# Optimization experiments

Measured on AMD Instinct MI355X. Metric: run time of the kernel, lower is better.

The kernel has to match this reference:

```python
import jax, jax.numpy as jnp
import numpy as np

NUM_GRAPHS = 512  # number of distinct graph ids in batch


def _gcn_agg(x, batch):
    # mm(block_full_adj, x) == per-graph sum broadcast back to nodes
    sums = jax.ops.segment_sum(x, batch, num_segments=NUM_GRAPHS)
    return sums[batch]


def setup_inputs() -> dict:
    key = jax.random.key(0)
    ks = jax.random.split(key, 8)
    N, D = 100000, 128
    H = 2 * D
    x = jax.random.normal(ks[0], (N, D), dtype=jnp.float32)
    batch = jnp.sort(jax.random.randint(ks[1], (N,), 0, NUM_GRAPHS)).astype(jnp.int64)
    s = 0.05
    W1 = jax.random.normal(ks[2], (D, H), dtype=jnp.float32) * s
    b1 = jax.random.normal(ks[3], (H,), dtype=jnp.float32) * s
    W2 = jax.random.normal(ks[4], (H, H), dtype=jnp.float32) * s
    b2 = jax.random.normal(ks[5], (H,), dtype=jnp.float32) * s
    Wc = jax.random.normal(ks[6], (H, 1), dtype=jnp.float32) * s
    bc = jax.random.normal(ks[7], (1,), dtype=jnp.float32) * s
    return {"x": x, "batch": batch, "W1": W1, "b1": b1, "W2": W2, "b2": b2, "Wc": Wc, "bc": bc}


def reference(x, batch, W1, b1, W2, b2, Wc, bc):
    h = jax.nn.relu(_gcn_agg(x, batch) @ W1 + b1)          # GCN layer 1
    h = jax.nn.relu(_gcn_agg(h, batch) @ W2 + b2)          # GCN layer 2
    c = h @ Wc + bc                                         # confidence head
    sp = jax.nn.softplus(c)
    return sp / (1.0 + sp)
```

## Files before the change

kernel.cpp:

```cpp
#include <hip/hip_runtime.h>
#include <math.h>

#define NUM_GRAPHS 512
#define D 128
#define HDIM 256

__global__ __launch_bounds__(256) void graph_mlp(
    const float* __restrict__ x,
    const int*   __restrict__ batch32,
    const float* __restrict__ W1, const float* __restrict__ b1,
    const float* __restrict__ W2, const float* __restrict__ b2,
    const float* __restrict__ Wc, const float* __restrict__ bc,
    float* __restrict__ cval, int* __restrict__ flagOut, int N)
{
    const int g   = blockIdx.x;
    const int tid = threadIdx.x;

    __shared__ int    sIs64;
    __shared__ int    sStart, sEnd;
    __shared__ float4 part[256];
    __shared__ float  sS[D];
    __shared__ float  sH[HDIM];
    __shared__ float  sRed[4];
    __shared__ int    sWave[4];

    {
        int cap = N < 8192 ? N : 8192;
        int local = 0x7fffffff;
        for (int i = tid; i < cap; i += 256) {
            if (batch32[i] != 0) { local = i; break; }
        }
        for (int off = 32; off > 0; off >>= 1)
            local = min(local, __shfl_down(local, off, 64));
        if ((tid & 63) == 0) sWave[tid >> 6] = local;
        __syncthreads();
        if (tid == 0) {
            int j = min(min(sWave[0], sWave[1]), min(sWave[2], sWave[3]));
            int is64 = 0;
            if (j != 0x7fffffff && j + 1 < N && batch32[j + 1] == 0) is64 = 1;
            sIs64 = is64;
            if (g == 0) *flagOut = is64;
        }
        __syncthreads();
    }
    const int is64 = sIs64;
    const long long* batch64 = (const long long*)batch32;

    if (tid < 2) {
        int target = g + tid;
        int lo = 0, hi = N;
        while (lo < hi) {
            int m = (lo + hi) >> 1;
            long long v = is64 ? batch64[m] : (long long)batch32[m];
            if (v < (long long)target) lo = m + 1; else hi = m;
        }
        if (tid == 0) sStart = lo; else sEnd = lo;
    }
    __syncthreads();
    const int start = sStart, end = sEnd;
    const float cnt = (float)(end - start);

    const int r  = tid >> 5;
    const int c4 = tid & 31;
    float4 acc = make_float4(0.f, 0.f, 0.f, 0.f);
    const float4* x4 = (const float4*)x;
    for (int row = start + r; row < end; row += 8) {
        float4 v = x4[row * 32 + c4];
        acc.x += v.x; acc.y += v.y; acc.z += v.z; acc.w += v.w;
    }
    part[tid] = acc;
    __syncthreads();
    for (int s = 4; s >= 1; s >>= 1) {
        if (r < s) {
            float4 o = part[tid + s * 32];
            float4 m = part[tid];
            m.x += o.x; m.y += o.y; m.z += o.z; m.w += o.w;
            part[tid] = m;
        }
        __syncthreads();
    }
    if (tid < 32) {
        float4 v = part[tid];
        sS[tid * 4 + 0] = v.x;
        sS[tid * 4 + 1] = v.y;
        sS[tid * 4 + 2] = v.z;
        sS[tid * 4 + 3] = v.w;
    }
    __syncthreads();

    float a1 = b1[tid];
    #pragma unroll 8
    for (int k = 0; k < D; ++k)
        a1 = fmaf(sS[k], W1[k * HDIM + tid], a1);
    sH[tid] = fmaxf(a1, 0.f) * cnt;
    __syncthreads();

    float a2 = b2[tid];
    #pragma unroll 8
    for (int k = 0; k < HDIM; ++k)
        a2 = fmaf(sH[k], W2[k * HDIM + tid], a2);
    float h2 = fmaxf(a2, 0.f);
    float v = h2 * Wc[tid];
    for (int off = 32; off > 0; off >>= 1)
        v += __shfl_down(v, off, 64);
    if ((tid & 63) == 0) sRed[tid >> 6] = v;
    __syncthreads();
    if (tid == 0) {
        float cc = sRed[0] + sRed[1] + sRed[2] + sRed[3] + bc[0];
        float m  = fmaxf(cc, 0.f);
        float sp = m + log1pf(expf(-fabsf(cc)));
        cval[g] = sp / (1.f + sp);
    }
}

__global__ __launch_bounds__(256) void scatter_out(
    const int* __restrict__ batch32, const int* __restrict__ flag,
    const float* __restrict__ cval, float* __restrict__ out, int N)
{
    const int is64 = *flag;
    const long long* batch64 = (const long long*)batch32;
    int i = blockIdx.x * 256 + threadIdx.x;
    if (i < N) {
        int g = is64 ? (int)batch64[i] : batch32[i];
        out[i] = cval[g];
    }
}

extern "C" void kernel_launch(void* const* d_in, const int* in_sizes, int n_in,
                              void* d_out, int out_size, void* d_ws, size_t ws_size,
                              hipStream_t stream)
{
    const float* x   = (const float*)d_in[0];
    const int*   bat = (const int*)d_in[1];
    const float* W1  = (const float*)d_in[2];
    const float* b1  = (const float*)d_in[3];
    const float* W2  = (const float*)d_in[4];
    const float* b2  = (const float*)d_in[5];
    const float* Wc  = (const float*)d_in[6];
    const float* bc  = (const float*)d_in[7];
    float* out = (float*)d_out;
    const int N = in_sizes[0] / D;

    float* cval = (float*)d_ws;
    int*   flag = (int*)((char*)d_ws + NUM_GRAPHS * sizeof(float));

    graph_mlp<<<NUM_GRAPHS, 256, 0, stream>>>(x, bat, W1, b1, W2, b2, Wc, bc,
                                              cval, flag, N);
    scatter_out<<<(N + 255) / 256, 256, 0, stream>>>(bat, flag, cval, out, N);
}
```

Measured before the change: 118.3 us.

## Split segment sum across blocks and batch MLP over several graphs per block

The segment sum now runs in its own kernel, which splits each graph's rows across K blocks to expose more parallelism and writes partial sums to workspace. A second kernel reduces the partials for GPB graphs per block, so each W1/W2 weight load is reused across four graphs, and writes the output directly over each graph's contiguous row range instead of using a separate scatter kernel. The probe that detects 32- versus 64-bit batch indices now scans fewer entries. The cost is a workspace round trip for the partials and fewer blocks (128) doing the MLP stage.

```diff
diff --git a/kernel.cpp b/kernel.cpp
--- a/kernel.cpp
+++ b/kernel.cpp
@@ -4,67 +4,75 @@
 #define NUM_GRAPHS 512
 #define D 128
 #define HDIM 256
-
-__global__ __launch_bounds__(256) void graph_mlp(
-    const float* __restrict__ x,
-    const int*   __restrict__ batch32,
-    const float* __restrict__ W1, const float* __restrict__ b1,
-    const float* __restrict__ W2, const float* __restrict__ b2,
-    const float* __restrict__ Wc, const float* __restrict__ bc,
-    float* __restrict__ cval, int* __restrict__ flagOut, int N)
-{
-    const int g   = blockIdx.x;
+#define K 4
+#define GPB 4
+
+#define DETECT_IS64(batch32, N, tid, sWave, sIs64)                         \
+    {                                                                      \
+        int cap = (N) < 1024 ? (N) : 1024;                                 \
+        int local = 0x7fffffff;                                            \
+        for (int i = (tid); i < cap; i += 256)                             \
+            if ((batch32)[i] != 0) { local = i; break; }                   \
+        for (int off = 32; off > 0; off >>= 1)                             \
+            local = min(local, __shfl_down(local, off, 64));               \
+        if (((tid) & 63) == 0) (sWave)[(tid) >> 6] = local;                \
+        __syncthreads();                                                   \
+        if ((tid) == 0) {                                                  \
+            int j = min(min((sWave)[0], (sWave)[1]),                       \
+                        min((sWave)[2], (sWave)[3]));                      \
+            (sIs64) = (j != 0x7fffffff && j + 1 < (N) &&                   \
+                       (batch32)[j + 1] == 0) ? 1 : 0;                     \
+        }                                                                  \
+        __syncthreads();                                                   \
+    }
+
+__device__ __forceinline__ int lower_bound_g(const int* batch32, int is64,
+                                             int N, int target)
+{
+    const long long* batch64 = (const long long*)batch32;
+    int lo = 0, hi = N;
+    while (lo < hi) {
+        int m = (lo + hi) >> 1;
+        long long v = is64 ? batch64[m] : (long long)batch32[m];
+        if (v < (long long)target) lo = m + 1; else hi = m;
+    }
+    return lo;
+}
+
+__global__ __launch_bounds__(256) void seg_sum(
+    const float* __restrict__ x, const int* __restrict__ batch32,
+    float4* __restrict__ partial4, int N)
+{
+    const int blk = blockIdx.x;
+    const int g   = blk / K;
+    const int k   = blk % K;
     const int tid = threadIdx.x;
 
     __shared__ int    sIs64;
+    __shared__ int    sWave[4];
     __shared__ int    sStart, sEnd;
     __shared__ float4 part[256];
-    __shared__ float  sS[D];
-    __shared__ float  sH[HDIM];
-    __shared__ float  sRed[4];
-    __shared__ int    sWave[4];
-
-    {
-        int cap = N < 8192 ? N : 8192;
-        int local = 0x7fffffff;
-        for (int i = tid; i < cap; i += 256) {
-            if (batch32[i] != 0) { local = i; break; }
-        }
-        for (int off = 32; off > 0; off >>= 1)
-            local = min(local, __shfl_down(local, off, 64));
-        if ((tid & 63) == 0) sWave[tid >> 6] = local;
-        __syncthreads();
-        if (tid == 0) {
-            int j = min(min(sWave[0], sWave[1]), min(sWave[2], sWave[3]));
-            int is64 = 0;
-            if (j != 0x7fffffff && j + 1 < N && batch32[j + 1] == 0) is64 = 1;
-            sIs64 = is64;
-            if (g == 0) *flagOut = is64;
-        }
-        __syncthreads();
-    }
+
+    DETECT_IS64(batch32, N, tid, sWave, sIs64);
     const int is64 = sIs64;
-    const long long* batch64 = (const long long*)batch32;
 
     if (tid < 2) {
-        int target = g + tid;
-        int lo = 0, hi = N;
-        while (lo < hi) {
-            int m = (lo + hi) >> 1;
-            long long v = is64 ? batch64[m] : (long long)batch32[m];
-            if (v < (long long)target) lo = m + 1; else hi = m;
-        }
+        int lo = lower_bound_g(batch32, is64, N, g + tid);
         if (tid == 0) sStart = lo; else sEnd = lo;
     }
     __syncthreads();
+
     const int start = sStart, end = sEnd;
-    const float cnt = (float)(end - start);
+    const int n   = end - start;
+    const int per = (n + K - 1) / K;
+    const int r0  = start + k * per;
+    const int r1  = min(r0 + per, end);
 
     const int r  = tid >> 5;
     const int c4 = tid & 31;
     float4 acc = make_float4(0.f, 0.f, 0.f, 0.f);
     const float4* x4 = (const float4*)x;
-    for (int row = start + r; row < end; row += 8) {
+    for (int row = r0 + r; row < r1; row += 8) {
         float4 v = x4[row * 32 + c4];
         acc.x += v.x; acc.y += v.y; acc.z += v.z; acc.w += v.w;
     }
@@ -79,50 +87,103 @@
         }
         __syncthreads();
     }
-    if (tid < 32) {
-        float4 v = part[tid];
-        sS[tid * 4 + 0] = v.x;
-        sS[tid * 4 + 1] = v.y;
-        sS[tid * 4 + 2] = v.z;
-        sS[tid * 4 + 3] = v.w;
-    }
-    __syncthreads();
-
-    float a1 = b1[tid];
-    #pragma unroll 8
-    for (int k = 0; k < D; ++k)
-        a1 = fmaf(sS[k], W1[k * HDIM + tid], a1);
-    sH[tid] = fmaxf(a1, 0.f) * cnt;
-    __syncthreads();
-
-    float a2 = b2[tid];
-    #pragma unroll 8
-    for (int k = 0; k < HDIM; ++k)
-        a2 = fmaf(sH[k], W2[k * HDIM + tid], a2);
-    float h2 = fmaxf(a2, 0.f);
-    float v = h2 * Wc[tid];
-    for (int off = 32; off > 0; off >>= 1)
-        v += __shfl_down(v, off, 64);
-    if ((tid & 63) == 0) sRed[tid >> 6] = v;
-    __syncthreads();
-    if (tid == 0) {
-        float cc = sRed[0] + sRed[1] + sRed[2] + sRed[3] + bc[0];
+    if (tid < 32)
+        partial4[blk * 32 + tid] = part[tid];
+}
+
+__global__ __launch_bounds__(256) void mlp_scatter(
+    const float* __restrict__ partial, const int* __restrict__ batch32,
+    const float* __restrict__ W1, const float* __restrict__ b1,
+    const float* __restrict__ W2, const float* __restrict__ b2,
+    const float* __restrict__ Wc, const float* __restrict__ bc,
+    float* __restrict__ out, int N)
+{
+    const int g0  = blockIdx.x * GPB;
+    const int tid = threadIdx.x;
+
+    __shared__ int   sIs64;
+    __shared__ int   sWave[4];
+    __shared__ int   sBound[GPB + 1];
+    __shared__ float sS[GPB][D];
+    __shared__ float sH[GPB][HDIM];
+    __shared__ float sRed[4][GPB];
+    __shared__ float sCval[GPB];
+
+    DETECT_IS64(batch32, N, tid, sWave, sIs64);
+    const int is64 = sIs64;
+
+    if (tid <= GPB)
+        sBound[tid] = lower_bound_g(batch32, is64, N, g0 + tid);
+    __syncthreads();
+
+    if (tid < D) {
+        #pragma unroll
+        for (int j = 0; j < GPB; ++j) {
+            float s = 0.f;
+            #pragma unroll
+            for (int k = 0; k < K; ++k)
+                s += partial[((g0 + j) * K + k) * D + tid];
+            sS[j][tid] = s;
+        }
+    }
+    __syncthreads();
+
+    float a1[GPB];
+    {
+        float bb = b1[tid];
+        #pragma unroll
+        for (int j = 0; j < GPB; ++j) a1[j] = bb;
+    }
+    for (int k = 0; k < D; ++k) {
+        float w = W1[k * HDIM + tid];
+        #pragma unroll
+        for (int j = 0; j < GPB; ++j) a1[j] = fmaf(sS[j][k], w, a1[j]);
+    }
+    #pragma unroll
+    for (int j = 0; j < GPB; ++j) {
+        float cnt = (float)(sBound[j + 1] - sBound[j]);
+        sH[j][tid] = fmaxf(a1[j], 0.f) * cnt;
+    }
+    __syncthreads();
+
+    float a2[GPB];
+    {
+        float bb = b2[tid];
+        #pragma unroll
+        for (int j = 0; j < GPB; ++j) a2[j] = bb;
+    }
+    for (int k = 0; k < HDIM; ++k) {
+        float w = W2[k * HDIM + tid];
+        #pragma unroll
+        for (int j = 0; j < GPB; ++j) a2[j] = fmaf(sH[j][k], w, a2[j]);
+    }
+    float wc = Wc[tid];
+    float v[GPB];
+    #pragma unroll
+    for (int j = 0; j < GPB; ++j) v[j] = fmaxf(a2[j], 0.f) * wc;
+    for (int off = 32; off > 0; off >>= 1) {
+        #pragma unroll
+        for (int j = 0; j < GPB; ++j) v[j] += __shfl_down(v[j], off, 64);
+    }
+    if ((tid & 63) == 0) {
+        #pragma unroll
+        for (int j = 0; j < GPB; ++j) sRed[tid >> 6][j] = v[j];
+    }
+    __syncthreads();
+    if (tid < GPB) {
+        float cc = sRed[0][tid] + sRed[1][tid] + sRed[2][tid] + sRed[3][tid]
+                 + bc[0];
         float m  = fmaxf(cc, 0.f);
         float sp = m + log1pf(expf(-fabsf(cc)));
-        cval[g] = sp / (1.f + sp);
-    }
-}
-
-__global__ __launch_bounds__(256) void scatter_out(
-    const int* __restrict__ batch32, const int* __restrict__ flag,
-    const float* __restrict__ cval, float* __restrict__ out, int N)
-{
-    const int is64 = *flag;
-    const long long* batch64 = (const long long*)batch32;
-    int i = blockIdx.x * 256 + threadIdx.x;
-    if (i < N) {
-        int g = is64 ? (int)batch64[i] : batch32[i];
-        out[i] = cval[g];
+        sCval[tid] = sp / (1.f + sp);
+    }
+    __syncthreads();
+
+    #pragma unroll
+    for (int j = 0; j < GPB; ++j) {
+        float val = sCval[j];
+        for (int i = sBound[j] + tid; i < sBound[j + 1]; i += 256)
+            out[i] = val;
     }
 }
 
@@ -141,10 +202,10 @@
     float* out = (float*)d_out;
     const int N = in_sizes[0] / D;
 
-    float* cval = (float*)d_ws;
-    int*   flag = (int*)((char*)d_ws + NUM_GRAPHS * sizeof(float));
-
-    graph_mlp<<<NUM_GRAPHS, 256, 0, stream>>>(x, bat, W1, b1, W2, b2, Wc, bc,
-                                              cval, flag, N);
-    scatter_out<<<(N + 255) / 256, 256, 0, stream>>>(bat, flag, cval, out, N);
-}
+    float* partial = (float*)d_ws;
+
+    seg_sum<<<NUM_GRAPHS * K, 256, 0, stream>>>(x, bat, (float4*)partial, N);
+    mlp_scatter<<<NUM_GRAPHS / GPB, 256, 0, stream>>>(partial, bat,
+                                                      W1, b1, W2, b2, Wc, bc,
+                                                      out, N);
+}
```

Result: slower. 126.1 us (+6.6%).
